# Kernel tuning notes

Measured on AMD Instinct MI355X. Metric: run time of the kernel, lower is better.

## Reference

```python
import jax, jax.numpy as jnp
import numpy as np

VOCAB, EMBED, HIDDEN, LAYERS = 32000, 256, 512, 2
B, T = 8, 512


def setup_inputs() -> dict:
    key = jax.random.key(0)
    ks = jax.random.split(key, 12)
    s_e = 1.0 / np.sqrt(EMBED)
    s_h = 1.0 / np.sqrt(HIDDEN)
    inp = {
        "input_ids": jax.random.randint(ks[0], (B, T), 0, VOCAB),
        "emb": jax.random.normal(ks[1], (VOCAB, EMBED), jnp.float32),
        # layer 0: input size EMBED
        "W_ih0": jax.random.uniform(ks[2], (4 * HIDDEN, EMBED), jnp.float32, -s_h, s_h),
        "W_hh0": jax.random.uniform(ks[3], (4 * HIDDEN, HIDDEN), jnp.float32, -s_h, s_h),
        "b_ih0": jax.random.uniform(ks[4], (4 * HIDDEN,), jnp.float32, -s_h, s_h),
        "b_hh0": jax.random.uniform(ks[5], (4 * HIDDEN,), jnp.float32, -s_h, s_h),
        # layer 1: input size HIDDEN
        "W_ih1": jax.random.uniform(ks[6], (4 * HIDDEN, HIDDEN), jnp.float32, -s_h, s_h),
        "W_hh1": jax.random.uniform(ks[7], (4 * HIDDEN, HIDDEN), jnp.float32, -s_h, s_h),
        "b_ih1": jax.random.uniform(ks[8], (4 * HIDDEN,), jnp.float32, -s_h, s_h),
        "b_hh1": jax.random.uniform(ks[9], (4 * HIDDEN,), jnp.float32, -s_h, s_h),
        "W_fc": jax.random.uniform(ks[10], (VOCAB, HIDDEN), jnp.float32, -s_h, s_h),
        "b_fc": jax.random.uniform(ks[11], (VOCAB,), jnp.float32, -s_h, s_h),
    }
    return inp


def _lstm_layer(x, W_ih, W_hh, b_ih, b_hh):
    # x: [B, T, D]; PyTorch gate order: i, f, g, o
    Bsz = x.shape[0]
    H = W_hh.shape[1]
    # precompute input contributions for all timesteps (one big GEMM)
    xg = jnp.einsum('btd,gd->btg', x, W_ih) + b_ih + b_hh  # [B, T, 4H]
    xg = xg.swapaxes(0, 1)  # time-major [T, B, 4H]

    def step(carry, xg_t):
        h, c = carry
        g = xg_t + h @ W_hh.T
        i, f, gg, o = jnp.split(g, 4, axis=-1)
        i = jax.nn.sigmoid(i)
        f = jax.nn.sigmoid(f)
        gg = jnp.tanh(gg)
        o = jax.nn.sigmoid(o)
        c = f * c + i * gg
        h = o * jnp.tanh(c)
        return (h, c), h

    h0 = jnp.zeros((Bsz, H), x.dtype)
    c0 = jnp.zeros((Bsz, H), x.dtype)
    _, hs = jax.lax.scan(step, (h0, c0), xg)  # hs: [T, B, H]
    return hs.swapaxes(0, 1)  # [B, T, H]


def reference(input_ids, emb, W_ih0, W_hh0, b_ih0, b_hh0,
              W_ih1, W_hh1, b_ih1, b_hh1, W_fc, b_fc):
    x = emb[input_ids]                                   # [B, T, E]
    x = _lstm_layer(x, W_ih0, W_hh0, b_ih0, b_hh0)       # [B, T, H]
    x = _lstm_layer(x, W_ih1, W_hh1, b_ih1, b_hh1)       # [B, T, H]
    logits = jnp.einsum('bth,vh->btv', x, W_fc) + b_fc   # [B, T, V]
    return logits
```

## Files before the change

### kernel.cpp

```cpp
#include <hip/hip_runtime.h>

typedef unsigned short u16;
typedef unsigned int   u32;
typedef unsigned long long u64;
typedef __attribute__((ext_vector_type(8))) short  short8;
typedef __attribute__((ext_vector_type(4))) float  floatx4;

__device__ __forceinline__ u16 f2bf(float f){
  u32 x = __float_as_uint(f);
  x += 0x7fffu + ((x >> 16) & 1u);
  return (u16)(x >> 16);
}
__device__ __forceinline__ u32 pk(float a, float b){
  return (u32)f2bf(a) | ((u32)f2bf(b) << 16);
}

#define TM 128
#define TN 128
#define BK 32
#define LDK 40

__global__ __launch_bounds__(256) void k_gemm(
    const void* __restrict__ Av, int a_f32, const int* __restrict__ a_rows,
    const float* __restrict__ B,
    const float* __restrict__ bias1, const float* __restrict__ bias2,
    float* __restrict__ outC,
    int M, int N, int K)
{
  __shared__ u16 As[TM][LDK];
  __shared__ u16 Bs[TN][LDK];
  const int tid  = threadIdx.x;
  const int n0   = blockIdx.x * TN;
  const int m0   = blockIdx.y * TM;
  const int wave = tid >> 6;
  const int lane = tid & 63;
  const int quad = lane >> 4;
  const int l16  = lane & 15;
  const int wm   = (wave >> 1) * 64;
  const int wn   = (wave & 1) * 64;

  const int srow = tid >> 1;
  const int scol = (tid & 1) * 16;
  int am = m0 + srow;
  if (a_rows) am = a_rows[am];
  const float* apf = (const float*)Av + (long)am * K + scol;
  const u16*   aph = (const u16*)Av + (long)am * K + scol;
  const float* bpf = B + (long)(n0 + srow) * K + scol;

  floatx4 acc[4][4] = {};

  for (int k0 = 0; k0 < K; k0 += BK){
    float4 b0 = *(const float4*)(bpf + k0);
    float4 b1 = *(const float4*)(bpf + k0 + 4);
    float4 b2 = *(const float4*)(bpf + k0 + 8);
    float4 b3 = *(const float4*)(bpf + k0 + 12);
    uint4 aS0, aS1;
    if (a_f32){
      float4 a0 = *(const float4*)(apf + k0);
      float4 a1 = *(const float4*)(apf + k0 + 4);
      float4 a2 = *(const float4*)(apf + k0 + 8);
      float4 a3 = *(const float4*)(apf + k0 + 12);
      aS0 = make_uint4(pk(a0.x,a0.y), pk(a0.z,a0.w), pk(a1.x,a1.y), pk(a1.z,a1.w));
      aS1 = make_uint4(pk(a2.x,a2.y), pk(a2.z,a2.w), pk(a3.x,a3.y), pk(a3.z,a3.w));
    } else {
      aS0 = *(const uint4*)(aph + k0);
      aS1 = *(const uint4*)(aph + k0 + 8);
    }
    uint4 bS0 = make_uint4(pk(b0.x,b0.y), pk(b0.z,b0.w), pk(b1.x,b1.y), pk(b1.z,b1.w));
    uint4 bS1 = make_uint4(pk(b2.x,b2.y), pk(b2.z,b2.w), pk(b3.x,b3.y), pk(b3.z,b3.w));
    __syncthreads();
    *(uint4*)&As[srow][scol]     = aS0;
    *(uint4*)&As[srow][scol + 8] = aS1;
    *(uint4*)&Bs[srow][scol]     = bS0;
    *(uint4*)&Bs[srow][scol + 8] = bS1;
    __syncthreads();
    short8 af[4], bfg[4];
    #pragma unroll
    for (int mt = 0; mt < 4; mt++) af[mt]  = *(const short8*)&As[wm + mt*16 + l16][quad*8];
    #pragma unroll
    for (int nt = 0; nt < 4; nt++) bfg[nt] = *(const short8*)&Bs[wn + nt*16 + l16][quad*8];
    #pragma unroll
    for (int mt = 0; mt < 4; mt++)
      #pragma unroll
      for (int nt = 0; nt < 4; nt++)
        acc[mt][nt] = __builtin_amdgcn_mfma_f32_16x16x32_bf16(af[mt], bfg[nt], acc[mt][nt], 0, 0, 0);
  }

  #pragma unroll
  for (int nt = 0; nt < 4; nt++){
    const int col = n0 + wn + nt*16 + l16;
    float bias = bias1[col];
    if (bias2) bias += bias2[col];
    #pragma unroll
    for (int mt = 0; mt < 4; mt++){
      #pragma unroll
      for (int r = 0; r < 4; r++){
        const int row = m0 + wm + mt*16 + quad*4 + r;
        outC[(long)row * N + col] = acc[mt][nt][r] + bias;
      }
    }
  }
}

__global__ __launch_bounds__(256, 1) void k_scan(
    const float* __restrict__ xg,
    const float* __restrict__ Whh,
    u16*        __restrict__ h_hist,
    float*      __restrict__ hbuf,
    int*        __restrict__ cnt)
{
  const int tid   = threadIdx.x;
  const int b     = blockIdx.x & 7;
  const int chunk = blockIdx.x >> 3;
  const int c0    = chunk * 16;
  const int rr    = tid >> 2;
  const int g     = rr >> 4;
  const int jj    = rr & 15;
  const int p     = tid & 3;
  const int nrow  = g * 512 + c0 + jj;

  __shared__ __align__(16) float h_lds[512];
  __shared__ float gates[64];
  __shared__ float c_lds[16];
  if (tid < 16) c_lds[tid] = 0.f;

  float4 w[32];
  const float4* wgp = (const float4*)(Whh + (long)nrow * 512 + p * 128);
  #pragma unroll
  for (int i = 0; i < 32; i++) w[i] = wgp[i];

  int* cnt_b = cnt + b * 32;
  const long xgbase = (long)b * 512 * 2048;
  int target = 0;

  for (int t = 0; t < 512; t++){
    float xgv = 0.f;
    if (p == 0) xgv = xg[xgbase + (long)t * 2048 + nrow];
    if (t > 0){
      const u64* hsrc = (const u64*)(hbuf + (((t - 1) & 1) * 8 + b) * 512);
      u64 v = __hip_atomic_load(hsrc + tid, __ATOMIC_RELAXED, __HIP_MEMORY_SCOPE_AGENT);
      ((u64*)h_lds)[tid] = v;
    }
    __syncthreads();

    float s = 0.f;
    if (t > 0){
      const float* hp = h_lds + p * 128;
      #pragma unroll
      for (int i = 0; i < 32; i++){
        float4 h4 = *(const float4*)(hp + i * 4);
        s += w[i].x * h4.x + w[i].y * h4.y + w[i].z * h4.z + w[i].w * h4.w;
      }
    }
    s += __shfl_xor(s, 1);
    s += __shfl_xor(s, 2);

    if (p == 0){
      float gv = xgv + s;
      gv = (g == 2) ? tanhf(gv) : 1.f / (1.f + __expf(-gv));
      gates[rr] = gv;
    }
    __syncthreads();

    if (tid < 16){
      float iv = gates[tid], fv = gates[16 + tid], gg = gates[32 + tid], ov = gates[48 + tid];
      float c = fv * c_lds[tid] + iv * gg;
      c_lds[tid] = c;
      float h = ov * tanhf(c);
      __hip_atomic_store(hbuf + ((t & 1) * 8 + b) * 512 + c0 + tid, h,
                         __ATOMIC_RELAXED, __HIP_MEMORY_SCOPE_AGENT);
      h_hist[(long)(b * 512 + t) * 512 + c0 + tid] = f2bf(h);
    }
    __syncthreads();

    target += 32;
    if (tid == 0){
      __hip_atomic_fetch_add(cnt_b, 1, __ATOMIC_RELEASE, __HIP_MEMORY_SCOPE_AGENT);
      while (__hip_atomic_load(cnt_b, __ATOMIC_ACQUIRE, __HIP_MEMORY_SCOPE_AGENT) < target){
        __builtin_amdgcn_s_sleep(1);
      }
    }
    __syncthreads();
  }
}

__global__ void k_init(int* cnt){ cnt[threadIdx.x] = 0; }

extern "C" void kernel_launch(void* const* d_in, const int* in_sizes, int n_in,
                              void* d_out, int out_size, void* d_ws, size_t ws_size,
                              hipStream_t stream)
{
  const int*   ids  = (const int*)d_in[0];
  const float* emb  = (const float*)d_in[1];
  const float* Wih0 = (const float*)d_in[2];
  const float* Whh0 = (const float*)d_in[3];
  const float* bih0 = (const float*)d_in[4];
  const float* bhh0 = (const float*)d_in[5];
  const float* Wih1 = (const float*)d_in[6];
  const float* Whh1 = (const float*)d_in[7];
  const float* bih1 = (const float*)d_in[8];
  const float* bhh1 = (const float*)d_in[9];
  const float* Wfc  = (const float*)d_in[10];
  const float* bfc  = (const float*)d_in[11];
  float* out = (float*)d_out;

  char* ws = (char*)d_ws;
  float* xg   = (float*)(ws);
  u16*   h0   = (u16*) (ws + (size_t)33554432);
  u16*   h1   = (u16*) (ws + (size_t)37748736);
  float* hbuf = (float*)(ws + (size_t)41943040);
  int*   cnt  = (int*)  (ws + (size_t)41943040 + 32768);

  k_init<<<dim3(1), dim3(1024), 0, stream>>>(cnt);

  k_gemm<<<dim3(16, 32), dim3(256), 0, stream>>>(
      (const void*)emb, 1, ids, Wih0, bih0, bhh0, xg, 4096, 2048, 256);

  k_scan<<<dim3(256), dim3(256), 0, stream>>>(xg, Whh0, h0, hbuf, cnt);

  k_gemm<<<dim3(16, 32), dim3(256), 0, stream>>>(
      (const void*)h0, 0, (const int*)nullptr, Wih1, bih1, bhh1, xg, 4096, 2048, 512);

  k_scan<<<dim3(256), dim3(256), 0, stream>>>(xg, Whh1, h1, hbuf, cnt + 256);

  k_gemm<<<dim3(250, 32), dim3(256), 0, stream>>>(
      (const void*)h1, 0, (const int*)nullptr, Wfc, bfc, (const float*)nullptr,
      out, 4096, 32000, 512);
}
```

Before: 9.399 ms.

## Fuse both LSTM layer scans into one wavefront-pipelined persistent kernel

Replaces the two sequential scan kernels and the layer-1 input GEMM with a single 512-block kernel. Layer-1 blocks trail layer-0 by one timestep, computing their input projection in-loop from register-resident W_ih1 and the bf16 layer-0 history, with progress tracked through a done counter. The intent is to overlap the two recurrences and drop one GEMM and one launch. In exchange it doubles register pressure (two 128-float weight slices per thread with two blocks per CU), adds cross-layer spin-waits, and rotates the LDS read order per lane to avoid bank conflicts; correctness depends on all 512 blocks being co-resident.

```diff
diff --git a/kernel.cpp b/kernel.cpp
--- a/kernel.cpp
+++ b/kernel.cpp
@@ -102,16 +102,23 @@
   }
 }
 
-__global__ __launch_bounds__(256, 1) void k_scan(
+__global__ __launch_bounds__(256, 2) void k_scan2(
     const float* __restrict__ xg,
-    const float* __restrict__ Whh,
-    u16*        __restrict__ h_hist,
+    const float* __restrict__ Whh0,
+    const float* __restrict__ Wih1,
+    const float* __restrict__ Whh1,
+    const float* __restrict__ bih1,
+    const float* __restrict__ bhh1,
+    u16*        __restrict__ h0h,
+    u16*        __restrict__ h1h,
     float*      __restrict__ hbuf,
     int*        __restrict__ cnt)
 {
   const int tid   = threadIdx.x;
-  const int b     = blockIdx.x & 7;
-  const int chunk = blockIdx.x >> 3;
+  const int layer = blockIdx.x >> 8;
+  const int idx   = blockIdx.x & 255;
+  const int b     = idx & 7;
+  const int chunk = idx >> 3;
   const int c0    = chunk * 16;
   const int rr    = tid >> 2;
   const int g     = rr >> 4;
@@ -120,24 +127,59 @@
   const int nrow  = g * 512 + c0 + jj;
 
   __shared__ __align__(16) float h_lds[512];
+  __shared__ __align__(16) float x_lds[512];
   __shared__ float gates[64];
   __shared__ float c_lds[16];
   if (tid < 16) c_lds[tid] = 0.f;
 
+  const float* Whh = layer ? Whh1 : Whh0;
   float4 w[32];
-  const float4* wgp = (const float4*)(Whh + (long)nrow * 512 + p * 128);
-  #pragma unroll
-  for (int i = 0; i < 32; i++) w[i] = wgp[i];
-
-  int* cnt_b = cnt + b * 32;
-  const long xgbase = (long)b * 512 * 2048;
+  {
+    const float4* wp = (const float4*)(Whh + (long)nrow * 512 + p * 128);
+    #pragma unroll
+    for (int i = 0; i < 32; i++) w[i] = wp[(i + p) & 31];
+    #pragma unroll
+    for (int i = 0; i < 32; i++)
+      asm volatile("" : "+v"(w[i].x), "+v"(w[i].y), "+v"(w[i].z), "+v"(w[i].w));
+  }
+  float4 wx[32];
+  float bias = 0.f;
+  if (layer){
+    const float4* wp = (const float4*)(Wih1 + (long)nrow * 512 + p * 128);
+    #pragma unroll
+    for (int i = 0; i < 32; i++) wx[i] = wp[(i + p) & 31];
+    #pragma unroll
+    for (int i = 0; i < 32; i++)
+      asm volatile("" : "+v"(wx[i].x), "+v"(wx[i].y), "+v"(wx[i].z), "+v"(wx[i].w));
+    bias = bih1[nrow] + bhh1[nrow];
+  }
+
+  int* cnt_me = cnt + layer * 256 + b * 32;
+  int* done0  = cnt + 512 + b * 32;
+  const long xgbase   = (long)b * 512 * 2048;
+  const long histbase = (long)b * 512 * 512;
   int target = 0;
+
+  if (layer){
+    if (tid == 0){
+      while (__hip_atomic_load(done0, __ATOMIC_ACQUIRE, __HIP_MEMORY_SCOPE_AGENT) < 1)
+        __builtin_amdgcn_s_sleep(1);
+    }
+    __syncthreads();
+  }
 
   for (int t = 0; t < 512; t++){
     float xgv = 0.f;
-    if (p == 0) xgv = xg[xgbase + (long)t * 2048 + nrow];
+    if (layer){
+      u32 pr = __hip_atomic_load((const u32*)(h0h + histbase + (long)t * 512) + tid,
+                                 __ATOMIC_RELAXED, __HIP_MEMORY_SCOPE_AGENT);
+      x_lds[2*tid]     = __uint_as_float((pr & 0xffffu) << 16);
+      x_lds[2*tid + 1] = __uint_as_float(pr & 0xffff0000u);
+    } else if (p == 0){
+      xgv = xg[xgbase + (long)t * 2048 + nrow];
+    }
     if (t > 0){
-      const u64* hsrc = (const u64*)(hbuf + (((t - 1) & 1) * 8 + b) * 512);
+      const u64* hsrc = (const u64*)(hbuf + ((layer*2 + ((t-1) & 1)) * 8 + b) * 512);
       u64 v = __hip_atomic_load(hsrc + tid, __ATOMIC_RELAXED, __HIP_MEMORY_SCOPE_AGENT);
       ((u64*)h_lds)[tid] = v;
     }
@@ -148,15 +190,23 @@
       const float* hp = h_lds + p * 128;
       #pragma unroll
       for (int i = 0; i < 32; i++){
-        float4 h4 = *(const float4*)(hp + i * 4);
+        float4 h4 = *(const float4*)(hp + (((i + p) & 31) << 2));
         s += w[i].x * h4.x + w[i].y * h4.y + w[i].z * h4.z + w[i].w * h4.w;
+      }
+    }
+    if (layer){
+      const float* xp = x_lds + p * 128;
+      #pragma unroll
+      for (int i = 0; i < 32; i++){
+        float4 h4 = *(const float4*)(xp + (((i + p) & 31) << 2));
+        s += wx[i].x * h4.x + wx[i].y * h4.y + wx[i].z * h4.z + wx[i].w * h4.w;
       }
     }
     s += __shfl_xor(s, 1);
     s += __shfl_xor(s, 2);
 
     if (p == 0){
-      float gv = xgv + s;
+      float gv = (layer ? bias : xgv) + s;
       gv = (g == 2) ? tanhf(gv) : 1.f / (1.f + __expf(-gv));
       gates[rr] = gv;
     }
@@ -167,18 +217,30 @@
       float c = fv * c_lds[tid] + iv * gg;
       c_lds[tid] = c;
       float h = ov * tanhf(c);
-      __hip_atomic_store(hbuf + ((t & 1) * 8 + b) * 512 + c0 + tid, h,
+      __hip_atomic_store(hbuf + ((layer*2 + (t & 1)) * 8 + b) * 512 + c0 + tid, h,
                          __ATOMIC_RELAXED, __HIP_MEMORY_SCOPE_AGENT);
-      h_hist[(long)(b * 512 + t) * 512 + c0 + tid] = f2bf(h);
-    }
-    __syncthreads();
+      if (layer){
+        h1h[histbase + (long)t * 512 + c0 + tid] = f2bf(h);
+      } else {
+        float hn = __shfl_down(h, 1);
+        if (!(tid & 1))
+          __hip_atomic_store((u32*)(h0h + histbase + (long)t * 512 + c0 + tid),
+                             pk(h, hn), __ATOMIC_RELAXED, __HIP_MEMORY_SCOPE_AGENT);
+      }
+    }
 
     target += 32;
     if (tid == 0){
-      __hip_atomic_fetch_add(cnt_b, 1, __ATOMIC_RELEASE, __HIP_MEMORY_SCOPE_AGENT);
-      while (__hip_atomic_load(cnt_b, __ATOMIC_ACQUIRE, __HIP_MEMORY_SCOPE_AGENT) < target){
+      __hip_atomic_fetch_add(cnt_me, 1, __ATOMIC_RELEASE, __HIP_MEMORY_SCOPE_AGENT);
+      for (;;){
+        bool ok = __hip_atomic_load(cnt_me, __ATOMIC_ACQUIRE, __HIP_MEMORY_SCOPE_AGENT) >= target;
+        if (ok && layer && t < 511)
+          ok = __hip_atomic_load(done0, __ATOMIC_ACQUIRE, __HIP_MEMORY_SCOPE_AGENT) >= t + 2;
+        if (ok) break;
         __builtin_amdgcn_s_sleep(1);
       }
+      if (!layer && chunk == 0)
+        __hip_atomic_store(done0, t + 1, __ATOMIC_RELEASE, __HIP_MEMORY_SCOPE_AGENT);
     }
     __syncthreads();
   }
@@ -206,24 +268,20 @@
 
   char* ws = (char*)d_ws;
   float* xg   = (float*)(ws);
-  u16*   h0   = (u16*) (ws + (size_t)33554432);
-  u16*   h1   = (u16*) (ws + (size_t)37748736);
+  u16*   h0h  = (u16*) (ws + (size_t)33554432);
+  u16*   h1h  = (u16*) (ws + (size_t)37748736);
   float* hbuf = (float*)(ws + (size_t)41943040);
-  int*   cnt  = (int*)  (ws + (size_t)41943040 + 32768);
+  int*   cnt  = (int*)  (ws + (size_t)41943040 + 65536);
 
   k_init<<<dim3(1), dim3(1024), 0, stream>>>(cnt);
 
   k_gemm<<<dim3(16, 32), dim3(256), 0, stream>>>(
       (const void*)emb, 1, ids, Wih0, bih0, bhh0, xg, 4096, 2048, 256);
 
-  k_scan<<<dim3(256), dim3(256), 0, stream>>>(xg, Whh0, h0, hbuf, cnt);
-
-  k_gemm<<<dim3(16, 32), dim3(256), 0, stream>>>(
-      (const void*)h0, 0, (const int*)nullptr, Wih1, bih1, bhh1, xg, 4096, 2048, 512);
-
-  k_scan<<<dim3(256), dim3(256), 0, stream>>>(xg, Whh1, h1, hbuf, cnt + 256);
+  k_scan2<<<dim3(512), dim3(256), 0, stream>>>(
+      xg, Whh0, Wih1, Whh1, bih1, bhh1, h0h, h1h, hbuf, cnt);
 
   k_gemm<<<dim3(250, 32), dim3(256), 0, stream>>>(
-      (const void*)h1, 0, (const int*)nullptr, Wfc, bfc, (const float*)nullptr,
+      (const void*)h1h, 0, (const int*)nullptr, Wfc, bfc, (const float*)nullptr,
       out, 4096, 32000, 512);
 }
```

Result: slower. 16.29 ms (+73.3%).
